# Kernel optimization log

Measured on AMD Instinct MI355X. Metric: run time of the kernel, lower is better.

Reference implementation:

```python
import jax, jax.numpy as jnp
import numpy as np

B = 128
N_ATOMS = 4096
NB, NA, NT = 4095, 4094, 4093
MAX_LEN = 5 * NT  # 20465, longest packed column (torsions)
EPS = 1e-8


def setup_inputs() -> dict:
    key = jax.random.key(0)
    ks = jax.random.split(key, 24)
    feats = jnp.zeros((B, MAX_LEN, 9), jnp.float32)
    # col 0: atom type ids
    atoms = jax.random.randint(ks[0], (B, N_ATOMS), 0, 6)
    # col 5: coords, flattened (N_ATOMS, 3)
    coords = jax.random.normal(ks[1], (B, N_ATOMS, 3), jnp.float32) * 5.0
    # col 6: bonds (i, j, type)
    bonds = jnp.stack([
        jax.random.randint(ks[2], (B, NB), 0, N_ATOMS),
        jax.random.randint(ks[3], (B, NB), 0, N_ATOMS),
        jax.random.randint(ks[4], (B, NB), 0, 15)], axis=-1)
    # col 7: angles (i, j, k, type)
    angles = jnp.stack([
        jax.random.randint(ks[5], (B, NA), 0, N_ATOMS),
        jax.random.randint(ks[6], (B, NA), 0, N_ATOMS),
        jax.random.randint(ks[7], (B, NA), 0, N_ATOMS),
        jax.random.randint(ks[8], (B, NA), 0, 13)], axis=-1)
    # col 8: torsions (i, j, k, l, type)
    tors = jnp.stack([
        jax.random.randint(ks[9], (B, NT), 0, N_ATOMS),
        jax.random.randint(ks[10], (B, NT), 0, N_ATOMS),
        jax.random.randint(ks[11], (B, NT), 0, N_ATOMS),
        jax.random.randint(ks[12], (B, NT), 0, N_ATOMS),
        jax.random.randint(ks[13], (B, NT), 0, 25)], axis=-1)
    feats = feats.at[:, :N_ATOMS, 0].set(atoms.astype(jnp.float32))
    feats = feats.at[:, :3 * N_ATOMS, 5].set(coords.reshape(B, -1))
    feats = feats.at[:, :3 * NB, 6].set(bonds.reshape(B, -1).astype(jnp.float32))
    feats = feats.at[:, :4 * NA, 7].set(angles.reshape(B, -1).astype(jnp.float32))
    feats = feats.at[:, :5 * NT, 8].set(tors.reshape(B, -1).astype(jnp.float32))
    lengths = jnp.tile(jnp.array(
        [[N_ATOMS, 0, 0, 0, 0, 3 * N_ATOMS, 3 * NB, 4 * NA, 5 * NT]],
        jnp.int32), (B, 1))
    bond_type = jnp.stack([jnp.ones(15), jax.random.uniform(ks[14], (15,), minval=1.0, maxval=2.0)], -1).astype(jnp.float32)
    angle_type = jnp.stack([jnp.ones(13), jax.random.uniform(ks[15], (13,), minval=1.0, maxval=3.0)], -1).astype(jnp.float32)
    tor_type = jnp.stack([jnp.ones(25), jax.random.uniform(ks[16], (25,), minval=0.0, maxval=3.14)], -1).astype(jnp.float32)
    multiplicity = jax.random.randint(ks[17], (25,), 1, 4)
    opt_pars = jax.random.uniform(ks[18], (47,), minval=0.5, maxval=1.5).astype(jnp.float32)
    return {"features": feats, "lengths": lengths, "bond_type": bond_type,
            "angle_type": angle_type, "tor_type": tor_type,
            "multiplicity": multiplicity, "opt_pars": opt_pars}


def _sample_energy(f, bond_type, angle_type, tor_type, multiplicity, opt_pars):
    coords = f[:3 * N_ATOMS, 5].reshape(-1, 3)                      # [N,3]
    bonds = f[:3 * NB, 6].astype(jnp.int32).reshape(-1, 3)          # [NB,3]
    angles = f[:4 * NA, 7].astype(jnp.int32).reshape(-1, 4)         # [NA,4]
    tors = f[:5 * NT, 8].astype(jnp.int32).reshape(-1, 5)           # [NT,5]

    # bonds: harmonic k*(r - r0)^2
    d = coords[bonds[:, 0]] - coords[bonds[:, 1]]
    r = jnp.sqrt(jnp.sum(d * d, -1) + EPS)
    pb = bond_type[bonds[:, 2]]
    e_bond = opt_pars[0] * jnp.sum(pb[:, 0] * (r - pb[:, 1]) ** 2)

    # angles: harmonic k*(theta - theta0)^2
    v1 = coords[angles[:, 0]] - coords[angles[:, 1]]
    v2 = coords[angles[:, 2]] - coords[angles[:, 1]]
    cosang = jnp.sum(v1 * v2, -1) / (
        jnp.sqrt(jnp.sum(v1 * v1, -1) + EPS) * jnp.sqrt(jnp.sum(v2 * v2, -1) + EPS))
    theta = jnp.arccos(jnp.clip(cosang, -1.0 + 1e-6, 1.0 - 1e-6))
    pa = angle_type[angles[:, 3]]
    e_ang = opt_pars[1] * jnp.sum(pa[:, 0] * (theta - pa[:, 1]) ** 2)

    # torsions: periodic k*(1 + cos(n*phi - delta))
    ci, cj, ck, cl = (coords[tors[:, m]] for m in range(4))
    b1, b2, b3 = cj - ci, ck - cj, cl - ck
    n1 = jnp.cross(b1, b2)
    n2 = jnp.cross(b2, b3)
    b2n = b2 / jnp.sqrt(jnp.sum(b2 * b2, -1, keepdims=True) + EPS)
    m1 = jnp.cross(n1, b2n)
    phi = jnp.arctan2(jnp.sum(m1 * n2, -1), jnp.sum(n1 * n2, -1))
    pt = tor_type[tors[:, 4]]
    n_mult = multiplicity[tors[:, 4]].astype(jnp.float32)
    e_tor = opt_pars[2] * jnp.sum(pt[:, 0] * (1.0 + jnp.cos(n_mult * phi - pt[:, 1])))

    return jnp.stack([e_bond, e_ang, e_tor])


def reference(features, lengths, bond_type, angle_type, tor_type, multiplicity, opt_pars):
    # lengths are uniform across batch (constants above); vmap over batch dim
    return jax.vmap(_sample_energy, in_axes=(0, None, None, None, None, None))(
        features, bond_type, angle_type, tor_type, multiplicity, opt_pars)
```

## Files before the change

### kernel.cpp

```cpp
#include <hip/hip_runtime.h>
#include <math.h>

#define BATCH    128
#define N_ATOMS  4096
#define NB       4095
#define NA       4094
#define NT       4093
#define FSTRIDE  184185
#define ROWS     20465
#define CROWS    12288
#define BROWS    12285
#define AROWS    16376
#define EPSV     1e-8f
#define THREADS  1024
#define WAVES    16
#define TPR      120
#define NTILES   171

typedef float float4a __attribute__((ext_vector_type(4), aligned(4)));


__global__ __launch_bounds__(THREADS, 1) void
local_energy_v12(const float* __restrict__ F,
                 const float* __restrict__ bond_type,
                 const float* __restrict__ angle_type,
                 const float* __restrict__ tor_type,
                 const int*   __restrict__ multiplicity,
                 const float* __restrict__ opt_pars,
                 float*       __restrict__ out)
{
    __shared__ float          scc[CROWS];
    __shared__ unsigned short sbB[BROWS + 1];
    __shared__ unsigned short sbA[AROWS];
    __shared__ unsigned short sbT[ROWS + 1];
    __shared__ float sbt[30], sat[26], stt[50], smu[25];
    __shared__ float sred[WAVES * 3];

    const int s   = blockIdx.x;
    const int tid = threadIdx.x;
    const int w   = tid >> 6;
    const int l   = tid & 63;
    const size_t sbase = (size_t)s * FSTRIDE;

    if (tid < 30)                      sbt[tid]       = bond_type[tid];
    else if (tid >= 32 && tid < 58)    sat[tid - 32]  = angle_type[tid - 32];
    else if (tid >= 64 && tid < 114)   stt[tid - 64]  = tor_type[tid - 64];
    else if (tid >= 128 && tid < 153)  smu[tid - 128] = (float)multiplicity[tid - 128];

    for (int t = w; t < NTILES; t += 2 * WAVES) {
        const int tb  = t + WAVES;
        const int R0a = TPR * t  + 2 * l;
        const int R0b = TPR * tb + 2 * l;
        const bool ok0a = (R0a     < ROWS);
        const bool ok1a = (R0a + 1 < ROWS);
        const bool ok0b = (R0b     < ROWS);
        const bool ok1b = (R0b + 1 < ROWS);
        const float* pa = F + sbase + (size_t)9 * R0a + 5;
        const float* pb = F + sbase + (size_t)9 * R0b + 5;
        float4a v0a, v1a, v0b, v1b;
        if (ok0a) v0a = *(const float4a*)(pa);
        if (ok1a) v1a = *(const float4a*)(pa + 9);
        if (ok0b) v0b = *(const float4a*)(pb);
        if (ok1b) v1b = *(const float4a*)(pb + 9);

        {
            const int R0 = R0a, R1 = R0a + 1;
            if (R1 < CROWS) {
                float2 c2; c2.x = v0a.x; c2.y = v1a.x;
                *(float2*)(scc + R0) = c2;
            }
            if (R1 < BROWS) {
                unsigned pk = (unsigned)(unsigned short)(int)v0a.y
                            | ((unsigned)(unsigned short)(int)v1a.y << 16);
                *(unsigned*)(sbB + R0) = pk;
            } else if (R0 < BROWS) {
                sbB[R0] = (unsigned short)(int)v0a.y;
            }
            if (R1 < AROWS) {
                unsigned pk = (unsigned)(unsigned short)(int)v0a.z
                            | ((unsigned)(unsigned short)(int)v1a.z << 16);
                *(unsigned*)(sbA + R0) = pk;
            }
            if (ok1a) {
                unsigned pk = (unsigned)(unsigned short)(int)v0a.w
                            | ((unsigned)(unsigned short)(int)v1a.w << 16);
                *(unsigned*)(sbT + R0) = pk;
            } else if (ok0a) {
                sbT[R0] = (unsigned short)(int)v0a.w;
            }
        }
        {
            const int R0 = R0b, R1 = R0b + 1;
            if (R1 < CROWS) {
                float2 c2; c2.x = v0b.x; c2.y = v1b.x;
                *(float2*)(scc + R0) = c2;
            }
            if (R1 < BROWS) {
                unsigned pk = (unsigned)(unsigned short)(int)v0b.y
                            | ((unsigned)(unsigned short)(int)v1b.y << 16);
                *(unsigned*)(sbB + R0) = pk;
            } else if (R0 < BROWS) {
                sbB[R0] = (unsigned short)(int)v0b.y;
            }
            if (R1 < AROWS) {
                unsigned pk = (unsigned)(unsigned short)(int)v0b.z
                            | ((unsigned)(unsigned short)(int)v1b.z << 16);
                *(unsigned*)(sbA + R0) = pk;
            }
            if (ok1b) {
                unsigned pk = (unsigned)(unsigned short)(int)v0b.w
                            | ((unsigned)(unsigned short)(int)v1b.w << 16);
                *(unsigned*)(sbT + R0) = pk;
            } else if (ok0b) {
                sbT[R0] = (unsigned short)(int)v0b.w;
            }
        }
    }
    __syncthreads();

    float eB = 0.f, eG = 0.f, eT = 0.f;
    for (int i = tid; i < NB; i += THREADS) {
        const int a0 = sbB[3 * i + 0];
        const int a1 = sbB[3 * i + 1];
        const int bt = sbB[3 * i + 2];
        const float dx = scc[3 * a0 + 0] - scc[3 * a1 + 0];
        const float dy = scc[3 * a0 + 1] - scc[3 * a1 + 1];
        const float dz = scc[3 * a0 + 2] - scc[3 * a1 + 2];
        const float r  = sqrtf(dx * dx + dy * dy + dz * dz + EPSV);
        const float t0 = r - sbt[bt * 2 + 1];
        eB += sbt[bt * 2 + 0] * t0 * t0;
    }
    for (int i = tid; i < NA; i += THREADS) {
        const int a0 = sbA[4 * i + 0];
        const int a1 = sbA[4 * i + 1];
        const int a2 = sbA[4 * i + 2];
        const int at = sbA[4 * i + 3];
        const float v1x = scc[3 * a0 + 0] - scc[3 * a1 + 0];
        const float v1y = scc[3 * a0 + 1] - scc[3 * a1 + 1];
        const float v1z = scc[3 * a0 + 2] - scc[3 * a1 + 2];
        const float v2x = scc[3 * a2 + 0] - scc[3 * a1 + 0];
        const float v2y = scc[3 * a2 + 1] - scc[3 * a1 + 1];
        const float v2z = scc[3 * a2 + 2] - scc[3 * a1 + 2];
        const float d12 = v1x * v2x + v1y * v2y + v1z * v2z;
        const float n1  = sqrtf(v1x * v1x + v1y * v1y + v1z * v1z + EPSV);
        const float n2  = sqrtf(v2x * v2x + v2y * v2y + v2z * v2z + EPSV);
        float cosang = d12 / (n1 * n2);
        cosang = fminf(fmaxf(cosang, -1.0f + 1e-6f), 1.0f - 1e-6f);
        const float t0 = acosf(cosang) - sat[at * 2 + 1];
        eG += sat[at * 2 + 0] * t0 * t0;
    }
    for (int i = tid; i < NT; i += THREADS) {
        const int ai = sbT[5 * i + 0];
        const int aj = sbT[5 * i + 1];
        const int ak = sbT[5 * i + 2];
        const int al = sbT[5 * i + 3];
        const int tt = sbT[5 * i + 4];
        const float b1x = scc[3*aj+0] - scc[3*ai+0];
        const float b1y = scc[3*aj+1] - scc[3*ai+1];
        const float b1z = scc[3*aj+2] - scc[3*ai+2];
        const float b2x = scc[3*ak+0] - scc[3*aj+0];
        const float b2y = scc[3*ak+1] - scc[3*aj+1];
        const float b2z = scc[3*ak+2] - scc[3*aj+2];
        const float b3x = scc[3*al+0] - scc[3*ak+0];
        const float b3y = scc[3*al+1] - scc[3*ak+1];
        const float b3z = scc[3*al+2] - scc[3*ak+2];
        const float n1x = b1y*b2z - b1z*b2y;
        const float n1y = b1z*b2x - b1x*b2z;
        const float n1z = b1x*b2y - b1y*b2x;
        const float n2x = b2y*b3z - b2z*b3y;
        const float n2y = b2z*b3x - b2x*b3z;
        const float n2z = b2x*b3y - b2y*b3x;
        const float inv = 1.0f / sqrtf(b2x*b2x + b2y*b2y + b2z*b2z + EPSV);
        const float bnx = b2x * inv, bny = b2y * inv, bnz = b2z * inv;
        const float m1x = n1y*bnz - n1z*bny;
        const float m1y = n1z*bnx - n1x*bnz;
        const float m1z = n1x*bny - n1y*bnx;
        const float phi = atan2f(m1x*n2x + m1y*n2y + m1z*n2z,
                                 n1x*n2x + n1y*n2y + n1z*n2z);
        eT += stt[tt * 2 + 0] * (1.0f + cosf(smu[tt] * phi - stt[tt * 2 + 1]));
    }

    for (int off = 32; off > 0; off >>= 1) {
        eB += __shfl_down(eB, off);
        eG += __shfl_down(eG, off);
        eT += __shfl_down(eT, off);
    }
    if (l == 0) {
        sred[w * 3 + 0] = eB;
        sred[w * 3 + 1] = eG;
        sred[w * 3 + 2] = eT;
    }
    __syncthreads();
    if (tid == 0) {
        float rB = 0.f, rG = 0.f, rT = 0.f;
        for (int i = 0; i < WAVES; ++i) {
            rB += sred[i * 3 + 0];
            rG += sred[i * 3 + 1];
            rT += sred[i * 3 + 2];
        }
        out[s * 3 + 0] = opt_pars[0] * rB;
        out[s * 3 + 1] = opt_pars[1] * rG;
        out[s * 3 + 2] = opt_pars[2] * rT;
    }
}

extern "C" void kernel_launch(void* const* d_in, const int* in_sizes, int n_in,
                              void* d_out, int out_size, void* d_ws, size_t ws_size,
                              hipStream_t stream) {
    const float* F            = (const float*)d_in[0];
    const float* bond_type    = (const float*)d_in[2];
    const float* angle_type   = (const float*)d_in[3];
    const float* tor_type     = (const float*)d_in[4];
    const int*   multiplicity = (const int*)  d_in[5];
    const float* opt_pars     = (const float*)d_in[6];
    float* out = (float*)d_out;

    local_energy_v12<<<dim3(BATCH), dim3(THREADS), 0, stream>>>(
        F, bond_type, angle_type, tor_type, multiplicity, opt_pars, out);
}
```

Before: 166.2 us.

## Stream whole feature rows as contiguous float4 chunks and scatter columns into LDS

The load phase now reads each sample's full 9-column feature buffer as contiguous float4 chunks instead of strided 16-byte reads starting at column 5. Each chunk's elements are routed to the coords, bond, angle or torsion arrays, with out-of-range lanes sent to dummy LDS slots so no branches are needed. This is meant to fully coalesce global loads and remove partial-row gathers, though it also reads the unused columns 0-4, about twice the bytes. LDS is repacked into one manually offset byte buffer.

```diff
diff --git a/kernel.cpp b/kernel.cpp
--- a/kernel.cpp
+++ b/kernel.cpp
@@ -11,17 +11,68 @@
 #define CROWS    12288
 #define BROWS    12285
 #define AROWS    16376
+#define TROWS    20465
 #define EPSV     1e-8f
 #define THREADS  1024
 #define WAVES    16
-#define TPR      120
-#define NTILES   171
+
+#define NCHUNK_FULL 46046
+
+#define OFF_SCC  0
+#define OFF_B    49152
+#define OFF_A    73728
+#define OFF_T    106480
+#define OFF_SBT  147412
+#define OFF_SAT  147532
+#define OFF_STT  147636
+#define OFF_SMU  147836
+#define OFF_SRED 147936
+#define OFF_D4   148128
+#define OFF_D2   148132
+#define LDS_SZ   148160
 
 typedef float float4a __attribute__((ext_vector_type(4), aligned(4)));
 
 
+__device__ __forceinline__ float sel4f(const float4a v, const int e) {
+    float r = v.w;
+    r = (e == 0) ? v.x : r;
+    r = (e == 1) ? v.y : r;
+    r = (e == 2) ? v.z : r;
+    return r;
+}
+
+__device__ __forceinline__ void extract_chunk(char* __restrict__ lds,
+                                              const float4a v,
+                                              const int r0, const int c0) {
+    {
+        const float cv = sel4f(v, 5 - c0);
+        const bool  ok = ((unsigned)(5 - c0) < 4u) && (r0 < CROWS);
+        const int   ad = ok ? (OFF_SCC + (r0 << 2)) : OFF_D4;
+        *(float*)(lds + ad) = cv;
+    }
+    {
+        const int  iv = (int)sel4f(v, 6 - c0);
+        const bool ok = ((unsigned)(6 - c0) < 4u) && (r0 < BROWS);
+        const int  ad = ok ? (OFF_B + (r0 << 1)) : OFF_D2;
+        *(unsigned short*)(lds + ad) = (unsigned short)iv;
+    }
+    {
+        const int  iv = (int)sel4f(v, 7 - c0);
+        const bool ok = ((unsigned)(7 - c0) < 4u) && (r0 < AROWS);
+        const int  ad = ok ? (OFF_A + (r0 << 1)) : OFF_D2;
+        *(unsigned short*)(lds + ad) = (unsigned short)iv;
+    }
+    {
+        const int  iv = (int)sel4f(v, 8 - c0);
+        const bool ok = ((unsigned)(8 - c0) < 4u);
+        const int  ad = ok ? (OFF_T + (r0 << 1)) : OFF_D2;
+        *(unsigned short*)(lds + ad) = (unsigned short)iv;
+    }
+}
+
 __global__ __launch_bounds__(THREADS, 1) void
-local_energy_v12(const float* __restrict__ F,
+local_energy_v15(const float* __restrict__ F,
                  const float* __restrict__ bond_type,
                  const float* __restrict__ angle_type,
                  const float* __restrict__ tor_type,
@@ -29,100 +80,60 @@
                  const float* __restrict__ opt_pars,
                  float*       __restrict__ out)
 {
-    __shared__ float          scc[CROWS];
-    __shared__ unsigned short sbB[BROWS + 1];
-    __shared__ unsigned short sbA[AROWS];
-    __shared__ unsigned short sbT[ROWS + 1];
-    __shared__ float sbt[30], sat[26], stt[50], smu[25];
-    __shared__ float sred[WAVES * 3];
+    __shared__ __align__(16) char LDSM[LDS_SZ];
+    char* lds = LDSM;
 
     const int s   = blockIdx.x;
     const int tid = threadIdx.x;
     const int w   = tid >> 6;
     const int l   = tid & 63;
-    const size_t sbase = (size_t)s * FSTRIDE;
+    const float* Fb = F + (size_t)s * FSTRIDE;
+
+    float* sbt = (float*)(lds + OFF_SBT);
+    float* sat = (float*)(lds + OFF_SAT);
+    float* stt = (float*)(lds + OFF_STT);
+    float* smu = (float*)(lds + OFF_SMU);
+    float* srd = (float*)(lds + OFF_SRED);
 
     if (tid < 30)                      sbt[tid]       = bond_type[tid];
     else if (tid >= 32 && tid < 58)    sat[tid - 32]  = angle_type[tid - 32];
     else if (tid >= 64 && tid < 114)   stt[tid - 64]  = tor_type[tid - 64];
     else if (tid >= 128 && tid < 153)  smu[tid - 128] = (float)multiplicity[tid - 128];
 
-    for (int t = w; t < NTILES; t += 2 * WAVES) {
-        const int tb  = t + WAVES;
-        const int R0a = TPR * t  + 2 * l;
-        const int R0b = TPR * tb + 2 * l;
-        const bool ok0a = (R0a     < ROWS);
-        const bool ok1a = (R0a + 1 < ROWS);
-        const bool ok0b = (R0b     < ROWS);
-        const bool ok1b = (R0b + 1 < ROWS);
-        const float* pa = F + sbase + (size_t)9 * R0a + 5;
-        const float* pb = F + sbase + (size_t)9 * R0b + 5;
-        float4a v0a, v1a, v0b, v1b;
-        if (ok0a) v0a = *(const float4a*)(pa);
-        if (ok1a) v1a = *(const float4a*)(pa + 9);
-        if (ok0b) v0b = *(const float4a*)(pb);
-        if (ok1b) v1b = *(const float4a*)(pb + 9);
-
-        {
-            const int R0 = R0a, R1 = R0a + 1;
-            if (R1 < CROWS) {
-                float2 c2; c2.x = v0a.x; c2.y = v1a.x;
-                *(float2*)(scc + R0) = c2;
-            }
-            if (R1 < BROWS) {
-                unsigned pk = (unsigned)(unsigned short)(int)v0a.y
-                            | ((unsigned)(unsigned short)(int)v1a.y << 16);
-                *(unsigned*)(sbB + R0) = pk;
-            } else if (R0 < BROWS) {
-                sbB[R0] = (unsigned short)(int)v0a.y;
-            }
-            if (R1 < AROWS) {
-                unsigned pk = (unsigned)(unsigned short)(int)v0a.z
-                            | ((unsigned)(unsigned short)(int)v1a.z << 16);
-                *(unsigned*)(sbA + R0) = pk;
-            }
-            if (ok1a) {
-                unsigned pk = (unsigned)(unsigned short)(int)v0a.w
-                            | ((unsigned)(unsigned short)(int)v1a.w << 16);
-                *(unsigned*)(sbT + R0) = pk;
-            } else if (ok0a) {
-                sbT[R0] = (unsigned short)(int)v0a.w;
-            }
+    int r0 = (4 * tid) / 9;
+    int c0 = 4 * tid - 9 * r0;
+
+    for (int j = 0; j < 44; j += 2) {
+        const int ci0 = tid + (j << 10);
+        const float4a v0 = *(const float4a*)(Fb + 4 * ci0);
+        const float4a v1 = *(const float4a*)(Fb + 4 * ci0 + 4096);
+        extract_chunk(lds, v0, r0, c0);
+        { c0 += 1; r0 += 455; if (c0 == 9) { c0 = 0; r0 += 1; } }
+        extract_chunk(lds, v1, r0, c0);
+        { c0 += 1; r0 += 455; if (c0 == 9) { c0 = 0; r0 += 1; } }
+    }
+    {
+        const int ci = tid + 45056;
+        if (ci < NCHUNK_FULL) {
+            const float4a v = *(const float4a*)(Fb + 4 * ci);
+            extract_chunk(lds, v, r0, c0);
+        } else if (ci == NCHUNK_FULL) {
+            const float x = Fb[FSTRIDE - 1];
+            *(unsigned short*)(lds + OFF_T + (20464 << 1)) = (unsigned short)(int)x;
         }
-        {
-            const int R0 = R0b, R1 = R0b + 1;
-            if (R1 < CROWS) {
-                float2 c2; c2.x = v0b.x; c2.y = v1b.x;
-                *(float2*)(scc + R0) = c2;
-            }
-            if (R1 < BROWS) {
-                unsigned pk = (unsigned)(unsigned short)(int)v0b.y
-                            | ((unsigned)(unsigned short)(int)v1b.y << 16);
-                *(unsigned*)(sbB + R0) = pk;
-            } else if (R0 < BROWS) {
-                sbB[R0] = (unsigned short)(int)v0b.y;
-            }
-            if (R1 < AROWS) {
-                unsigned pk = (unsigned)(unsigned short)(int)v0b.z
-                            | ((unsigned)(unsigned short)(int)v1b.z << 16);
-                *(unsigned*)(sbA + R0) = pk;
-            }
-            if (ok1b) {
-                unsigned pk = (unsigned)(unsigned short)(int)v0b.w
-                            | ((unsigned)(unsigned short)(int)v1b.w << 16);
-                *(unsigned*)(sbT + R0) = pk;
-            } else if (ok0b) {
-                sbT[R0] = (unsigned short)(int)v0b.w;
-            }
-        }
     }
     __syncthreads();
+
+    const float*          scc = (const float*)(lds + OFF_SCC);
+    const unsigned short* pB  = (const unsigned short*)(lds + OFF_B);
+    const unsigned short* pA  = (const unsigned short*)(lds + OFF_A);
+    const unsigned short* pT  = (const unsigned short*)(lds + OFF_T);
 
     float eB = 0.f, eG = 0.f, eT = 0.f;
     for (int i = tid; i < NB; i += THREADS) {
-        const int a0 = sbB[3 * i + 0];
-        const int a1 = sbB[3 * i + 1];
-        const int bt = sbB[3 * i + 2];
+        const int a0 = pB[3 * i + 0];
+        const int a1 = pB[3 * i + 1];
+        const int bt = pB[3 * i + 2];
         const float dx = scc[3 * a0 + 0] - scc[3 * a1 + 0];
         const float dy = scc[3 * a0 + 1] - scc[3 * a1 + 1];
         const float dz = scc[3 * a0 + 2] - scc[3 * a1 + 2];
@@ -131,10 +142,10 @@
         eB += sbt[bt * 2 + 0] * t0 * t0;
     }
     for (int i = tid; i < NA; i += THREADS) {
-        const int a0 = sbA[4 * i + 0];
-        const int a1 = sbA[4 * i + 1];
-        const int a2 = sbA[4 * i + 2];
-        const int at = sbA[4 * i + 3];
+        const int a0 = pA[4 * i + 0];
+        const int a1 = pA[4 * i + 1];
+        const int a2 = pA[4 * i + 2];
+        const int at = pA[4 * i + 3];
         const float v1x = scc[3 * a0 + 0] - scc[3 * a1 + 0];
         const float v1y = scc[3 * a0 + 1] - scc[3 * a1 + 1];
         const float v1z = scc[3 * a0 + 2] - scc[3 * a1 + 2];
@@ -150,11 +161,11 @@
         eG += sat[at * 2 + 0] * t0 * t0;
     }
     for (int i = tid; i < NT; i += THREADS) {
-        const int ai = sbT[5 * i + 0];
-        const int aj = sbT[5 * i + 1];
-        const int ak = sbT[5 * i + 2];
-        const int al = sbT[5 * i + 3];
-        const int tt = sbT[5 * i + 4];
+        const int ai = pT[5 * i + 0];
+        const int aj = pT[5 * i + 1];
+        const int ak = pT[5 * i + 2];
+        const int al = pT[5 * i + 3];
+        const int tt = pT[5 * i + 4];
         const float b1x = scc[3*aj+0] - scc[3*ai+0];
         const float b1y = scc[3*aj+1] - scc[3*ai+1];
         const float b1z = scc[3*aj+2] - scc[3*ai+2];
@@ -186,17 +197,17 @@
         eT += __shfl_down(eT, off);
     }
     if (l == 0) {
-        sred[w * 3 + 0] = eB;
-        sred[w * 3 + 1] = eG;
-        sred[w * 3 + 2] = eT;
+        srd[w * 3 + 0] = eB;
+        srd[w * 3 + 1] = eG;
+        srd[w * 3 + 2] = eT;
     }
     __syncthreads();
     if (tid == 0) {
         float rB = 0.f, rG = 0.f, rT = 0.f;
         for (int i = 0; i < WAVES; ++i) {
-            rB += sred[i * 3 + 0];
-            rG += sred[i * 3 + 1];
-            rT += sred[i * 3 + 2];
+            rB += srd[i * 3 + 0];
+            rG += srd[i * 3 + 1];
+            rT += srd[i * 3 + 2];
         }
         out[s * 3 + 0] = opt_pars[0] * rB;
         out[s * 3 + 1] = opt_pars[1] * rG;
@@ -215,6 +226,6 @@
     const float* opt_pars     = (const float*)d_in[6];
     float* out = (float*)d_out;
 
-    local_energy_v12<<<dim3(BATCH), dim3(THREADS), 0, stream>>>(
+    local_energy_v15<<<dim3(BATCH), dim3(THREADS), 0, stream>>>(
         F, bond_type, angle_type, tor_type, multiplicity, opt_pars, out);
 }
```

New measurement: 163.4 us. No clear change (-1.7%).
